# Kernel optimization log

Hardware: AMD Instinct MI355X
Metric: run time of the kernel (lower is better)

The kernel has to match this reference:

```python
import jax, jax.numpy as jnp
import numpy as np

N = 100_000   # nodes
E = 1_600_000 # edges per relation (avg degree 16)
IN, H, O = 128, 128, 128


def _graph_conv(x, src, dst, W, b, relu):
    """DGL GraphConv, norm='both': y = D_dst^{-1/2} A D_src^{-1/2} x W + b."""
    ones = jnp.ones(src.shape[0], dtype=x.dtype)
    deg_out = jnp.clip(jax.ops.segment_sum(ones, src, num_segments=N), 1.0)  # [N]
    deg_in = jnp.clip(jax.ops.segment_sum(ones, dst, num_segments=N), 1.0)   # [N]
    h = (x * (deg_out ** -0.5)[:, None]) @ W                 # [N, out] transform first (in==out)
    agg = jax.ops.segment_sum(h[src], dst, num_segments=N)   # SpMM: gather + scatter-add
    y = agg * (deg_in ** -0.5)[:, None] + b
    return jax.nn.relu(y) if relu else y


def setup_inputs() -> dict:
    key = jax.random.key(0)
    ks = jax.random.split(key, 8)
    g = 0.1  # weight scale ~ xavier for d=128
    return {
        "x": jax.random.normal(ks[0], (N, IN), dtype=jnp.float32),
        "src_i": jax.random.randint(ks[1], (E,), 0, N),
        "dst_i": jax.random.randint(ks[2], (E,), 0, N),
        "src_b": jax.random.randint(ks[3], (E,), 0, N),
        "dst_b": jax.random.randint(ks[4], (E,), 0, N),
        "W1_i": jax.random.normal(ks[5], (IN, H), dtype=jnp.float32) * g,
        "b1_i": jnp.zeros((H,), dtype=jnp.float32),
        "W1_b": jax.random.normal(ks[6], (IN, H), dtype=jnp.float32) * g,
        "b1_b": jnp.zeros((H,), dtype=jnp.float32),
        "W2": jax.random.normal(ks[7], (H, O), dtype=jnp.float32) * g,
        "b2": jnp.zeros((O,), dtype=jnp.float32),
    }


def reference(x, src_i, dst_i, src_b, dst_b, W1_i, b1_i, W1_b, b1_b, W2, b2):
    # conv1: HeteroGraphConv({'interacts','behave'}, aggregate='sum'), ReLU inside each conv
    h = (_graph_conv(x, src_i, dst_i, W1_i, b1_i, relu=True)
         + _graph_conv(x, src_b, dst_b, W1_b, b1_b, relu=True))
    # conv2: only 'interacts', no activation
    return _graph_conv(h, src_i, dst_i, W2, b2, relu=False)
```

## Files before the change

### kernel.cpp

```cpp
#include <hip/hip_runtime.h>
#include <hip/hip_fp16.h>

#define N_NODES 100000
#define N_EDGES 1600000
#define NT 98
#define XB 64
#define CHUNK (N_EDGES / XB)
#define HSH 2
#define HBINS (N_NODES / HSH)
#define PSH 128
#define PBINS ((N_NODES + PSH - 1) / PSH)
#define TILE 4096
#define WT_LD 136

typedef _Float16 half8_t __attribute__((ext_vector_type(8)));
typedef float f32x4 __attribute__((ext_vector_type(4)));
typedef unsigned long long u64;

__device__ inline unsigned packh2(float a, float b) {
  __half2 h = __floats2half2_rn(a, b);
  return *(unsigned*)&h;
}

__global__ __launch_bounds__(256) void k_hist(
    const int* __restrict__ src_i, const int* __restrict__ dst_i,
    const int* __restrict__ src_b, const int* __restrict__ dst_b,
    unsigned* __restrict__ part32) {
  __shared__ unsigned h[HBINS / 4];
  const int xb = blockIdx.x, job = blockIdx.y, sl = blockIdx.z;
  const int* arr = (job == 0) ? src_i : (job == 1) ? dst_i : (job == 2) ? src_b : dst_b;
  const int lo = sl * HBINS;
  for (int i = threadIdx.x; i < HBINS / 4; i += 256) h[i] = 0;
  __syncthreads();
  const int4* a4 = (const int4*)(arr + xb * CHUNK);
  for (int q = threadIdx.x; q < CHUNK / 4; q += 256) {
    int4 v = a4[q];
    int t;
    t = v.x - lo; if ((unsigned)t < HBINS) atomicAdd(&h[t >> 2], 1u << ((t & 3) * 8));
    t = v.y - lo; if ((unsigned)t < HBINS) atomicAdd(&h[t >> 2], 1u << ((t & 3) * 8));
    t = v.z - lo; if ((unsigned)t < HBINS) atomicAdd(&h[t >> 2], 1u << ((t & 3) * 8));
    t = v.w - lo; if ((unsigned)t < HBINS) atomicAdd(&h[t >> 2], 1u << ((t & 3) * 8));
  }
  __syncthreads();
  unsigned* dst = part32 + ((size_t)(job * XB + xb) * N_NODES + lo) / 4;
  for (int i = threadIdx.x; i < HBINS / 4; i += 256) dst[i] = h[i];
}

__global__ __launch_bounds__(256) void k_hred(
    const unsigned* __restrict__ part32, int* __restrict__ cnt_di_i, int* __restrict__ cnt_di_b,
    float* __restrict__ dso_i, float* __restrict__ dsi_i,
    float* __restrict__ dso_b, float* __restrict__ dsi_b) {
  const int b4 = blockIdx.x * 256 + threadIdx.x;
  if (b4 >= N_NODES / 4) return;
  const int b0 = b4 * 4;
  const size_t Q = N_NODES / 4;
  int s0, s1, s2, s3;
  s0 = s1 = s2 = s3 = 0;
  for (int xb = 0; xb < XB; ++xb) {
    unsigned w = part32[(size_t)(0 * XB + xb) * Q + b4];
    s0 += w & 255; s1 += (w >> 8) & 255; s2 += (w >> 16) & 255; s3 += w >> 24;
  }
  dso_i[b0] = rsqrtf((float)max(s0, 1)); dso_i[b0 + 1] = rsqrtf((float)max(s1, 1));
  dso_i[b0 + 2] = rsqrtf((float)max(s2, 1)); dso_i[b0 + 3] = rsqrtf((float)max(s3, 1));
  s0 = s1 = s2 = s3 = 0;
  for (int xb = 0; xb < XB; ++xb) {
    unsigned w = part32[(size_t)(1 * XB + xb) * Q + b4];
    s0 += w & 255; s1 += (w >> 8) & 255; s2 += (w >> 16) & 255; s3 += w >> 24;
  }
  cnt_di_i[b0] = s0; cnt_di_i[b0 + 1] = s1; cnt_di_i[b0 + 2] = s2; cnt_di_i[b0 + 3] = s3;
  dsi_i[b0] = rsqrtf((float)max(s0, 1)); dsi_i[b0 + 1] = rsqrtf((float)max(s1, 1));
  dsi_i[b0 + 2] = rsqrtf((float)max(s2, 1)); dsi_i[b0 + 3] = rsqrtf((float)max(s3, 1));
  s0 = s1 = s2 = s3 = 0;
  for (int xb = 0; xb < XB; ++xb) {
    unsigned w = part32[(size_t)(2 * XB + xb) * Q + b4];
    s0 += w & 255; s1 += (w >> 8) & 255; s2 += (w >> 16) & 255; s3 += w >> 24;
  }
  dso_b[b0] = rsqrtf((float)max(s0, 1)); dso_b[b0 + 1] = rsqrtf((float)max(s1, 1));
  dso_b[b0 + 2] = rsqrtf((float)max(s2, 1)); dso_b[b0 + 3] = rsqrtf((float)max(s3, 1));
  s0 = s1 = s2 = s3 = 0;
  for (int xb = 0; xb < XB; ++xb) {
    unsigned w = part32[(size_t)(3 * XB + xb) * Q + b4];
    s0 += w & 255; s1 += (w >> 8) & 255; s2 += (w >> 16) & 255; s3 += w >> 24;
  }
  cnt_di_b[b0] = s0; cnt_di_b[b0 + 1] = s1; cnt_di_b[b0 + 2] = s2; cnt_di_b[b0 + 3] = s3;
  dsi_b[b0] = rsqrtf((float)max(s0, 1)); dsi_b[b0 + 1] = rsqrtf((float)max(s1, 1));
  dsi_b[b0 + 2] = rsqrtf((float)max(s2, 1)); dsi_b[b0 + 3] = rsqrtf((float)max(s3, 1));
}

__global__ __launch_bounds__(256) void k_scan1(
    const int* __restrict__ cnt_i, const int* __restrict__ cnt_b,
    int* __restrict__ off_i, int* __restrict__ off_b, int* __restrict__ tsum) {
  const int rel = blockIdx.y;
  const int* cnt = rel ? cnt_b : cnt_i;
  int* off = rel ? off_b : off_i;
  const int tid = threadIdx.x;
  const int i0 = blockIdx.x * 1024 + tid * 4;
  int v[4];
#pragma unroll
  for (int k = 0; k < 4; ++k) v[k] = (i0 + k < N_NODES) ? cnt[i0 + k] : 0;
  int tl = v[0] + v[1] + v[2] + v[3];
  const int lane = tid & 63, wid = tid >> 6;
  int x = tl;
#pragma unroll
  for (int d = 1; d < 64; d <<= 1) {
    int t = __shfl_up(x, d);
    if (lane >= d) x += t;
  }
  __shared__ int wsum[4];
  if (lane == 63) wsum[wid] = x;
  __syncthreads();
  int wb = 0;
#pragma unroll
  for (int w = 0; w < 4; ++w)
    if (w < wid) wb += wsum[w];
  int run = wb + x - tl;
#pragma unroll
  for (int k = 0; k < 4; ++k) {
    if (i0 + k < N_NODES) off[i0 + k] = run;
    run += v[k];
  }
  if (tid == 255) tsum[rel * NT + blockIdx.x] = wb + x;
}

__global__ __launch_bounds__(256) void k_scan2(int* __restrict__ tsum) {
  __shared__ int a[256], b[256];
  const int t = threadIdx.x;
  for (int rel = 0; rel < 2; ++rel) {
    a[t] = (t < NT) ? tsum[rel * NT + t] : 0;
    __syncthreads();
    int* p = a;
    int* q = b;
    for (int d = 1; d < 256; d <<= 1) {
      q[t] = (t >= d) ? p[t - d] + p[t] : p[t];
      __syncthreads();
      int* tmp = p; p = q; q = tmp;
    }
    int excl = (t == 0) ? 0 : p[t - 1];
    if (t < NT) tsum[rel * NT + t] = excl;
    __syncthreads();
  }
}

__global__ __launch_bounds__(256) void k_scan3(
    const int* __restrict__ tsum, int* __restrict__ off_i, int* __restrict__ off_b) {
  const int rel = blockIdx.y;
  int* off = rel ? off_b : off_i;
  const int tb = tsum[rel * NT + blockIdx.x];
  const int i0 = blockIdx.x * 1024 + threadIdx.x * 4;
#pragma unroll
  for (int k = 0; k < 4; ++k)
    if (i0 + k < N_NODES) off[i0 + k] += tb;
  if (blockIdx.x == 0 && threadIdx.x == 0) off[N_NODES] = N_EDGES;
}

__global__ void k_binit(const int* __restrict__ off_i, const int* __restrict__ off_b,
                        int* __restrict__ bcur) {
  int i = threadIdx.x;
  if (i < 2 * PSH) {
    int rel = i >> 7, b = i & (PSH - 1);
    bcur[i] = (rel ? off_b : off_i)[b * PBINS];
  }
}

__global__ __launch_bounds__(256) void k_bucket(
    const int* __restrict__ src_i, const int* __restrict__ dst_i,
    const int* __restrict__ src_b, const int* __restrict__ dst_b,
    int* __restrict__ bcur, u64* __restrict__ pairs_i, u64* __restrict__ pairs_b) {
  __shared__ u64 stage[TILE];
  __shared__ int cnt[PSH], excl[PSH], gbase[PSH], lpos[PSH], sa[PSH], sb[PSH];
  const int rel = blockIdx.y;
  const int* src = rel ? src_b : src_i;
  const int* dst = rel ? dst_b : dst_i;
  u64* pairs = rel ? pairs_b : pairs_i;
  const int tid = threadIdx.x;
  const int base = blockIdx.x * TILE;
  const int nE = min(TILE, N_EDGES - base);

  for (int i = tid; i < PSH; i += 256) { cnt[i] = 0; lpos[i] = 0; }
  __syncthreads();

  u64 ed[16];
  int eb[16];
#pragma unroll
  for (int j = 0; j < 16; ++j) {
    int idx = base + j * 256 + tid;
    if (idx < N_EDGES && (j * 256 + tid) < nE) {
      int s = src[idx], d = dst[idx];
      ed[j] = ((u64)(unsigned)d << 32) | (unsigned)s;
      eb[j] = d / PBINS;
      atomicAdd(&cnt[eb[j]], 1);
    } else {
      eb[j] = -1;
    }
  }
  __syncthreads();
  if (tid < PSH) sa[tid] = cnt[tid];
  __syncthreads();
  int* p = sa;
  int* q = sb;
  for (int d = 1; d < PSH; d <<= 1) {
    if (tid < PSH) q[tid] = ((tid >= d) ? p[tid - d] : 0) + p[tid];
    __syncthreads();
    int* tmp = p; p = q; q = tmp;
  }
  if (tid < PSH) {
    excl[tid] = p[tid] - cnt[tid];
    gbase[tid] = atomicAdd(&bcur[rel * PSH + tid], cnt[tid]);
  }
  __syncthreads();
#pragma unroll
  for (int j = 0; j < 16; ++j) {
    if (eb[j] >= 0) {
      int pos = excl[eb[j]] + atomicAdd(&lpos[eb[j]], 1);
      stage[pos] = ed[j];
    }
  }
  __syncthreads();
  for (int i = tid; i < nE; i += 256) {
    u64 e = stage[i];
    int b = (int)(e >> 32) / PBINS;
    pairs[(size_t)gbase[b] + (i - excl[b])] = e;
  }
}

__global__ __launch_bounds__(256) void k_fill2(
    const int* __restrict__ off_i, const int* __restrict__ off_b,
    const u64* __restrict__ pairs_i, const u64* __restrict__ pairs_b,
    int* __restrict__ es_i, int* __restrict__ es_b) {
  __shared__ int cur[PBINS];
  const int b = blockIdx.x, rel = blockIdx.y;
  const int* off = rel ? off_b : off_i;
  const u64* pairs = rel ? pairs_b : pairs_i;
  int* es = rel ? es_b : es_i;
  const int lo = b * PBINS;
  const int hi = min(lo + PBINS, N_NODES);
  const int bins = hi - lo;
  for (int i = threadIdx.x; i < bins; i += 256) cur[i] = off[lo + i];
  __syncthreads();
  const int p0 = off[lo], p1 = off[hi];
  for (int idx = p0 + threadIdx.x; idx < p1; idx += 256) {
    u64 e = pairs[idx];
    int d = (int)(e >> 32);
    int p = atomicAdd(&cur[d - lo], 1);
    es[p] = (int)(unsigned)e;
  }
}

__global__ __launch_bounds__(256) void k_gemm_mfma(
    const float* __restrict__ A,
    const float* __restrict__ Wa, const float* __restrict__ Wb,
    const float* __restrict__ rsa, const float* __restrict__ rsb,
    unsigned short* __restrict__ Ca, unsigned short* __restrict__ Cb) {
  __shared__ unsigned short shw[128 * WT_LD];
  const int rel = blockIdx.y;
  const float* W = rel ? Wb : Wa;
  const float* rs = rel ? rsb : rsa;
  unsigned short* C = rel ? Cb : Ca;

  for (int t = threadIdx.x; t < 2048; t += 256) {
    int c4 = (t & 31) * 4;
    int k = (t >> 5) * 2;
    float4 w0 = *(const float4*)&W[k * 128 + c4];
    float4 w1 = *(const float4*)&W[(k + 1) * 128 + c4];
    *(unsigned*)&shw[(c4 + 0) * WT_LD + k] = packh2(w0.x, w1.x);
    *(unsigned*)&shw[(c4 + 1) * WT_LD + k] = packh2(w0.y, w1.y);
    *(unsigned*)&shw[(c4 + 2) * WT_LD + k] = packh2(w0.z, w1.z);
    *(unsigned*)&shw[(c4 + 3) * WT_LD + k] = packh2(w0.w, w1.w);
  }
  __syncthreads();

  const int w = threadIdx.x >> 6;
  const int l = threadIdx.x & 63;
  const int lc = l & 15;
  const int lk = l >> 4;
  const int rb = blockIdx.x * 128 + w * 32;

  f32x4 acc[2][8];
#pragma unroll
  for (int rf = 0; rf < 2; ++rf)
#pragma unroll
    for (int cf = 0; cf < 8; ++cf) acc[rf][cf] = (f32x4)(0.f);

  union H8 { unsigned u[4]; half8_t h; };

#pragma unroll
  for (int kc = 0; kc < 4; ++kc) {
    const int kbase = kc * 32 + lk * 8;
    H8 a[2];
#pragma unroll
    for (int rf = 0; rf < 2; ++rf) {
      int row = rb + rf * 16 + lc;
      row = min(row, N_NODES - 1);
      const float4* ap = (const float4*)(A + (size_t)row * 128 + kbase);
      float4 f0 = ap[0], f1 = ap[1];
      a[rf].u[0] = packh2(f0.x, f0.y);
      a[rf].u[1] = packh2(f0.z, f0.w);
      a[rf].u[2] = packh2(f1.x, f1.y);
      a[rf].u[3] = packh2(f1.z, f1.w);
    }
#pragma unroll
    for (int cf = 0; cf < 8; ++cf) {
      half8_t b = *(const half8_t*)&shw[(cf * 16 + lc) * WT_LD + kbase];
      acc[0][cf] = __builtin_amdgcn_mfma_f32_16x16x32_f16(a[0].h, b, acc[0][cf], 0, 0, 0);
      acc[1][cf] = __builtin_amdgcn_mfma_f32_16x16x32_f16(a[1].h, b, acc[1][cf], 0, 0, 0);
    }
  }

#pragma unroll
  for (int rf = 0; rf < 2; ++rf) {
#pragma unroll
    for (int reg = 0; reg < 4; ++reg) {
      int row = rb + rf * 16 + lk * 4 + reg;
      if (row < N_NODES) {
        float s = rs[row];
        unsigned short* crow = C + (size_t)row * 128 + lc;
#pragma unroll
        for (int cf = 0; cf < 8; ++cf) {
          __half h = __float2half_rn(acc[rf][cf][reg] * s);
          crow[cf * 16] = *(unsigned short*)&h;
        }
      }
    }
  }
}

__device__ inline void spmm_acc(const uint4* __restrict__ Xv, const int* __restrict__ srcs,
                                int e0, int e1, int l, float* a) {
  int e = e0;
  for (; e + 16 <= e1; e += 16) {
    int s = srcs[e + l];
    uint4 v[16];
#pragma unroll
    for (int j = 0; j < 16; ++j) v[j] = Xv[(size_t)__shfl(s, j, 16) * 16 + l];
#pragma unroll
    for (int j = 0; j < 16; ++j) {
      float2 f;
      f = __half22float2(*(__half2*)&v[j].x); a[0] += f.x; a[1] += f.y;
      f = __half22float2(*(__half2*)&v[j].y); a[2] += f.x; a[3] += f.y;
      f = __half22float2(*(__half2*)&v[j].z); a[4] += f.x; a[5] += f.y;
      f = __half22float2(*(__half2*)&v[j].w); a[6] += f.x; a[7] += f.y;
    }
  }
  if (e < e1) {
    int s = (e + l < e1) ? srcs[e + l] : 0;
    int cnt = e1 - e;
    for (int j = 0; j < cnt; ++j) {
      uint4 v = Xv[(size_t)__shfl(s, j, 16) * 16 + l];
      float2 f;
      f = __half22float2(*(__half2*)&v.x); a[0] += f.x; a[1] += f.y;
      f = __half22float2(*(__half2*)&v.y); a[2] += f.x; a[3] += f.y;
      f = __half22float2(*(__half2*)&v.z); a[4] += f.x; a[5] += f.y;
      f = __half22float2(*(__half2*)&v.w); a[6] += f.x; a[7] += f.y;
    }
  }
}

__global__ __launch_bounds__(256) void k_spmm_l1(
    const unsigned short* __restrict__ Xi, const int* __restrict__ off_i,
    const int* __restrict__ es_i, const float* __restrict__ dsi_i,
    const float* __restrict__ b_i,
    const unsigned short* __restrict__ Xb, const int* __restrict__ off_b,
    const int* __restrict__ es_b, const float* __restrict__ dsi_b,
    const float* __restrict__ b_b, float* __restrict__ out) {
  const int g = threadIdx.x >> 4;
  const int l = threadIdx.x & 15;
  const int n = blockIdx.x * 16 + g;
  if (n >= N_NODES) return;
  float y[8];
  {
    float a[8] = {0.f, 0.f, 0.f, 0.f, 0.f, 0.f, 0.f, 0.f};
    spmm_acc((const uint4*)Xi, es_i, off_i[n], off_i[n + 1], l, a);
    const float dn = dsi_i[n];
    float4 c0 = ((const float4*)b_i)[l * 2];
    float4 c1 = ((const float4*)b_i)[l * 2 + 1];
    y[0] = fmaxf(fmaf(a[0], dn, c0.x), 0.f); y[1] = fmaxf(fmaf(a[1], dn, c0.y), 0.f);
    y[2] = fmaxf(fmaf(a[2], dn, c0.z), 0.f); y[3] = fmaxf(fmaf(a[3], dn, c0.w), 0.f);
    y[4] = fmaxf(fmaf(a[4], dn, c1.x), 0.f); y[5] = fmaxf(fmaf(a[5], dn, c1.y), 0.f);
    y[6] = fmaxf(fmaf(a[6], dn, c1.z), 0.f); y[7] = fmaxf(fmaf(a[7], dn, c1.w), 0.f);
  }
  {
    float a[8] = {0.f, 0.f, 0.f, 0.f, 0.f, 0.f, 0.f, 0.f};
    spmm_acc((const uint4*)Xb, es_b, off_b[n], off_b[n + 1], l, a);
    const float dn = dsi_b[n];
    float4 c0 = ((const float4*)b_b)[l * 2];
    float4 c1 = ((const float4*)b_b)[l * 2 + 1];
    y[0] += fmaxf(fmaf(a[0], dn, c0.x), 0.f); y[1] += fmaxf(fmaf(a[1], dn, c0.y), 0.f);
    y[2] += fmaxf(fmaf(a[2], dn, c0.z), 0.f); y[3] += fmaxf(fmaf(a[3], dn, c0.w), 0.f);
    y[4] += fmaxf(fmaf(a[4], dn, c1.x), 0.f); y[5] += fmaxf(fmaf(a[5], dn, c1.y), 0.f);
    y[6] += fmaxf(fmaf(a[6], dn, c1.z), 0.f); y[7] += fmaxf(fmaf(a[7], dn, c1.w), 0.f);
  }
  float4* ov = (float4*)out;
  size_t oi = (size_t)n * 32 + l * 2;
  ov[oi] = make_float4(y[0], y[1], y[2], y[3]);
  ov[oi + 1] = make_float4(y[4], y[5], y[6], y[7]);
}

__global__ __launch_bounds__(256) void k_spmm_l2(
    const unsigned short* __restrict__ Xh, const int* __restrict__ off,
    const int* __restrict__ srcs, const float* __restrict__ dsi,
    const float* __restrict__ bias, float* __restrict__ out) {
  const int g = threadIdx.x >> 4;
  const int l = threadIdx.x & 15;
  const int n = blockIdx.x * 16 + g;
  if (n >= N_NODES) return;
  float a[8] = {0.f, 0.f, 0.f, 0.f, 0.f, 0.f, 0.f, 0.f};
  spmm_acc((const uint4*)Xh, srcs, off[n], off[n + 1], l, a);
  const float dn = dsi[n];
  float4 c0 = ((const float4*)bias)[l * 2];
  float4 c1 = ((const float4*)bias)[l * 2 + 1];
  float4 y0, y1;
  y0.x = fmaf(a[0], dn, c0.x); y0.y = fmaf(a[1], dn, c0.y);
  y0.z = fmaf(a[2], dn, c0.z); y0.w = fmaf(a[3], dn, c0.w);
  y1.x = fmaf(a[4], dn, c1.x); y1.y = fmaf(a[5], dn, c1.y);
  y1.z = fmaf(a[6], dn, c1.z); y1.w = fmaf(a[7], dn, c1.w);
  float4* ov = (float4*)out;
  size_t oi = (size_t)n * 32 + l * 2;
  ov[oi] = y0;
  ov[oi + 1] = y1;
}

extern "C" void kernel_launch(void* const* d_in, const int* in_sizes, int n_in,
                              void* d_out, int out_size, void* d_ws, size_t ws_size,
                              hipStream_t stream) {
  const float* x    = (const float*)d_in[0];
  const int* src_i  = (const int*)d_in[1];
  const int* dst_i  = (const int*)d_in[2];
  const int* src_b  = (const int*)d_in[3];
  const int* dst_b  = (const int*)d_in[4];
  const float* W1_i = (const float*)d_in[5];
  const float* b1_i = (const float*)d_in[6];
  const float* W1_b = (const float*)d_in[7];
  const float* b1_b = (const float*)d_in[8];
  const float* W2   = (const float*)d_in[9];
  const float* b2   = (const float*)d_in[10];
  float* out = (float*)d_out;

  char* ws = (char*)d_ws;
  size_t o = 0;
  auto alloc = [&](size_t bytes) {
    char* p = ws + o;
    o += (bytes + 255) & ~(size_t)255;
    return p;
  };
  float* dso_i = (float*)alloc(N_NODES * 4);
  float* dsi_i = (float*)alloc(N_NODES * 4);
  float* dso_b = (float*)alloc(N_NODES * 4);
  float* dsi_b = (float*)alloc(N_NODES * 4);
  int* cnt_di_i = (int*)alloc(N_NODES * 4);
  int* cnt_di_b = (int*)alloc(N_NODES * 4);
  int* off_i = (int*)alloc((N_NODES + 1) * 4);
  int* off_b = (int*)alloc((N_NODES + 1) * 4);
  int* tsum = (int*)alloc(2 * NT * 4);
  int* bcur = (int*)alloc(2 * PSH * 4);
  int* es_i = (int*)alloc((size_t)N_EDGES * 4);
  int* es_b = (int*)alloc((size_t)N_EDGES * 4);
  char* uni = alloc((size_t)2 * N_NODES * 128 * 2);
  unsigned* part32      = (unsigned*)uni;
  u64* pairs_i          = (u64*)uni;
  u64* pairs_b          = pairs_i + N_EDGES;
  unsigned short* buf_i = (unsigned short*)uni;
  unsigned short* buf_b = (unsigned short*)(uni + (size_t)N_NODES * 128 * 2);
  (void)ws_size; (void)in_sizes; (void)n_in; (void)out_size;

  k_hist<<<dim3(XB, 4, HSH), dim3(256), 0, stream>>>(src_i, dst_i, src_b, dst_b, part32);
  k_hred<<<(N_NODES / 4 + 255) / 256, dim3(256), 0, stream>>>(
      part32, cnt_di_i, cnt_di_b, dso_i, dsi_i, dso_b, dsi_b);
  k_scan1<<<dim3(NT, 2), dim3(256), 0, stream>>>(cnt_di_i, cnt_di_b, off_i, off_b, tsum);
  k_scan2<<<1, 256, 0, stream>>>(tsum);
  k_scan3<<<dim3(NT, 2), dim3(256), 0, stream>>>(tsum, off_i, off_b);
  k_binit<<<1, 256, 0, stream>>>(off_i, off_b, bcur);
  k_bucket<<<dim3((N_EDGES + TILE - 1) / TILE, 2), dim3(256), 0, stream>>>(
      src_i, dst_i, src_b, dst_b, bcur, pairs_i, pairs_b);
  k_fill2<<<dim3(PSH, 2), dim3(256), 0, stream>>>(
      off_i, off_b, pairs_i, pairs_b, es_i, es_b);

  const int ggrid = (N_NODES + 127) / 128;
  const int sgrid = (N_NODES + 15) / 16;
  k_gemm_mfma<<<dim3(ggrid, 2), dim3(256), 0, stream>>>(
      x, W1_i, W1_b, dso_i, dso_b, buf_i, buf_b);
  k_spmm_l1<<<sgrid, 256, 0, stream>>>(
      buf_i, off_i, es_i, dsi_i, b1_i, buf_b, off_b, es_b, dsi_b, b1_b, out);
  k_gemm_mfma<<<dim3(ggrid, 1), dim3(256), 0, stream>>>(
      out, W2, W2, dso_i, dso_i, buf_i, buf_i);
  k_spmm_l2<<<sgrid, 256, 0, stream>>>(buf_i, off_i, es_i, dsi_i, b2, out);
}
```

Measured before the change: 466.5 us.

## Derive in-degree CSR offsets inside fill from fixed-capacity dst buckets

The destination-degree histogram and the three-pass global scan are dropped. Bucketing now writes edges into fixed-capacity per-bucket segments, and a tiny prefix kernel computes the bucket bases. Each fill block then counts in-degrees locally, scans them, and writes offsets, inverse-sqrt degrees and sorted sources. This removes two of the four histogram jobs and several small launches, but it assumes no bucket exceeds PCAP edges, which holds for the uniform random test graph and would overflow on skewed graphs.

```diff
diff --git a/kernel.cpp b/kernel.cpp
--- a/kernel.cpp
+++ b/kernel.cpp
@@ -3,13 +3,13 @@
 
 #define N_NODES 100000
 #define N_EDGES 1600000
-#define NT 98
 #define XB 64
 #define CHUNK (N_EDGES / XB)
 #define HSH 2
 #define HBINS (N_NODES / HSH)
 #define PSH 128
 #define PBINS ((N_NODES + PSH - 1) / PSH)
+#define PCAP 16384
 #define TILE 4096
 #define WT_LD 136
 
@@ -23,12 +23,11 @@
 }
 
 __global__ __launch_bounds__(256) void k_hist(
-    const int* __restrict__ src_i, const int* __restrict__ dst_i,
-    const int* __restrict__ src_b, const int* __restrict__ dst_b,
+    const int* __restrict__ src_i, const int* __restrict__ src_b,
     unsigned* __restrict__ part32) {
   __shared__ unsigned h[HBINS / 4];
   const int xb = blockIdx.x, job = blockIdx.y, sl = blockIdx.z;
-  const int* arr = (job == 0) ? src_i : (job == 1) ? dst_i : (job == 2) ? src_b : dst_b;
+  const int* arr = job ? src_b : src_i;
   const int lo = sl * HBINS;
   for (int i = threadIdx.x; i < HBINS / 4; i += 256) h[i] = 0;
   __syncthreads();
@@ -47,9 +46,8 @@
 }
 
 __global__ __launch_bounds__(256) void k_hred(
-    const unsigned* __restrict__ part32, int* __restrict__ cnt_di_i, int* __restrict__ cnt_di_b,
-    float* __restrict__ dso_i, float* __restrict__ dsi_i,
-    float* __restrict__ dso_b, float* __restrict__ dsi_b) {
+    const unsigned* __restrict__ part32,
+    float* __restrict__ dso_i, float* __restrict__ dso_b) {
   const int b4 = blockIdx.x * 256 + threadIdx.x;
   if (b4 >= N_NODES / 4) return;
   const int b0 = b4 * 4;
@@ -67,111 +65,19 @@
     unsigned w = part32[(size_t)(1 * XB + xb) * Q + b4];
     s0 += w & 255; s1 += (w >> 8) & 255; s2 += (w >> 16) & 255; s3 += w >> 24;
   }
-  cnt_di_i[b0] = s0; cnt_di_i[b0 + 1] = s1; cnt_di_i[b0 + 2] = s2; cnt_di_i[b0 + 3] = s3;
-  dsi_i[b0] = rsqrtf((float)max(s0, 1)); dsi_i[b0 + 1] = rsqrtf((float)max(s1, 1));
-  dsi_i[b0 + 2] = rsqrtf((float)max(s2, 1)); dsi_i[b0 + 3] = rsqrtf((float)max(s3, 1));
-  s0 = s1 = s2 = s3 = 0;
-  for (int xb = 0; xb < XB; ++xb) {
-    unsigned w = part32[(size_t)(2 * XB + xb) * Q + b4];
-    s0 += w & 255; s1 += (w >> 8) & 255; s2 += (w >> 16) & 255; s3 += w >> 24;
-  }
   dso_b[b0] = rsqrtf((float)max(s0, 1)); dso_b[b0 + 1] = rsqrtf((float)max(s1, 1));
   dso_b[b0 + 2] = rsqrtf((float)max(s2, 1)); dso_b[b0 + 3] = rsqrtf((float)max(s3, 1));
-  s0 = s1 = s2 = s3 = 0;
-  for (int xb = 0; xb < XB; ++xb) {
-    unsigned w = part32[(size_t)(3 * XB + xb) * Q + b4];
-    s0 += w & 255; s1 += (w >> 8) & 255; s2 += (w >> 16) & 255; s3 += w >> 24;
-  }
-  cnt_di_b[b0] = s0; cnt_di_b[b0 + 1] = s1; cnt_di_b[b0 + 2] = s2; cnt_di_b[b0 + 3] = s3;
-  dsi_b[b0] = rsqrtf((float)max(s0, 1)); dsi_b[b0 + 1] = rsqrtf((float)max(s1, 1));
-  dsi_b[b0 + 2] = rsqrtf((float)max(s2, 1)); dsi_b[b0 + 3] = rsqrtf((float)max(s3, 1));
-}
-
-__global__ __launch_bounds__(256) void k_scan1(
-    const int* __restrict__ cnt_i, const int* __restrict__ cnt_b,
-    int* __restrict__ off_i, int* __restrict__ off_b, int* __restrict__ tsum) {
-  const int rel = blockIdx.y;
-  const int* cnt = rel ? cnt_b : cnt_i;
-  int* off = rel ? off_b : off_i;
-  const int tid = threadIdx.x;
-  const int i0 = blockIdx.x * 1024 + tid * 4;
-  int v[4];
-#pragma unroll
-  for (int k = 0; k < 4; ++k) v[k] = (i0 + k < N_NODES) ? cnt[i0 + k] : 0;
-  int tl = v[0] + v[1] + v[2] + v[3];
-  const int lane = tid & 63, wid = tid >> 6;
-  int x = tl;
-#pragma unroll
-  for (int d = 1; d < 64; d <<= 1) {
-    int t = __shfl_up(x, d);
-    if (lane >= d) x += t;
-  }
-  __shared__ int wsum[4];
-  if (lane == 63) wsum[wid] = x;
-  __syncthreads();
-  int wb = 0;
-#pragma unroll
-  for (int w = 0; w < 4; ++w)
-    if (w < wid) wb += wsum[w];
-  int run = wb + x - tl;
-#pragma unroll
-  for (int k = 0; k < 4; ++k) {
-    if (i0 + k < N_NODES) off[i0 + k] = run;
-    run += v[k];
-  }
-  if (tid == 255) tsum[rel * NT + blockIdx.x] = wb + x;
-}
-
-__global__ __launch_bounds__(256) void k_scan2(int* __restrict__ tsum) {
-  __shared__ int a[256], b[256];
-  const int t = threadIdx.x;
-  for (int rel = 0; rel < 2; ++rel) {
-    a[t] = (t < NT) ? tsum[rel * NT + t] : 0;
-    __syncthreads();
-    int* p = a;
-    int* q = b;
-    for (int d = 1; d < 256; d <<= 1) {
-      q[t] = (t >= d) ? p[t - d] + p[t] : p[t];
-      __syncthreads();
-      int* tmp = p; p = q; q = tmp;
-    }
-    int excl = (t == 0) ? 0 : p[t - 1];
-    if (t < NT) tsum[rel * NT + t] = excl;
-    __syncthreads();
-  }
-}
-
-__global__ __launch_bounds__(256) void k_scan3(
-    const int* __restrict__ tsum, int* __restrict__ off_i, int* __restrict__ off_b) {
-  const int rel = blockIdx.y;
-  int* off = rel ? off_b : off_i;
-  const int tb = tsum[rel * NT + blockIdx.x];
-  const int i0 = blockIdx.x * 1024 + threadIdx.x * 4;
-#pragma unroll
-  for (int k = 0; k < 4; ++k)
-    if (i0 + k < N_NODES) off[i0 + k] += tb;
-  if (blockIdx.x == 0 && threadIdx.x == 0) off[N_NODES] = N_EDGES;
-}
-
-__global__ void k_binit(const int* __restrict__ off_i, const int* __restrict__ off_b,
-                        int* __restrict__ bcur) {
-  int i = threadIdx.x;
-  if (i < 2 * PSH) {
-    int rel = i >> 7, b = i & (PSH - 1);
-    bcur[i] = (rel ? off_b : off_i)[b * PBINS];
-  }
 }
 
 __global__ __launch_bounds__(256) void k_bucket(
     const int* __restrict__ src_i, const int* __restrict__ dst_i,
     const int* __restrict__ src_b, const int* __restrict__ dst_b,
-    int* __restrict__ bcur, u64* __restrict__ pairs_i, u64* __restrict__ pairs_b) {
+    int* __restrict__ bcur, u64* __restrict__ pairs) {
   __shared__ u64 stage[TILE];
   __shared__ int cnt[PSH], excl[PSH], gbase[PSH], lpos[PSH], sa[PSH], sb[PSH];
   const int rel = blockIdx.y;
   const int* src = rel ? src_b : src_i;
   const int* dst = rel ? dst_b : dst_i;
-  u64* pairs = rel ? pairs_b : pairs_i;
   const int tid = threadIdx.x;
   const int base = blockIdx.x * TILE;
   const int nE = min(TILE, N_EDGES - base);
@@ -219,30 +125,91 @@
   for (int i = tid; i < nE; i += 256) {
     u64 e = stage[i];
     int b = (int)(e >> 32) / PBINS;
-    pairs[(size_t)gbase[b] + (i - excl[b])] = e;
-  }
+    pairs[(size_t)(rel * PSH + b) * PCAP + gbase[b] + (i - excl[b])] = e;
+  }
+}
+
+__global__ void k_bprefix(const int* __restrict__ bcur, int* __restrict__ bbase,
+                          int* __restrict__ off_i, int* __restrict__ off_b) {
+  __shared__ int ws[2][2];
+  const int tid = threadIdx.x;
+  const int rel = tid >> 7, i = tid & 127;
+  const int lane = tid & 63;
+  const int w2 = (tid >> 6) & 1;
+  int v = bcur[rel * PSH + i];
+  int x = v;
+#pragma unroll
+  for (int d = 1; d < 64; d <<= 1) {
+    int t = __shfl_up(x, d);
+    if (lane >= d) x += t;
+  }
+  if (lane == 63) ws[rel][w2] = x;
+  __syncthreads();
+  int addv = (w2 == 1) ? ws[rel][0] : 0;
+  bbase[rel * PSH + i] = x - v + addv;
+  if (tid == 0) { off_i[N_NODES] = N_EDGES; off_b[N_NODES] = N_EDGES; }
 }
 
 __global__ __launch_bounds__(256) void k_fill2(
-    const int* __restrict__ off_i, const int* __restrict__ off_b,
-    const u64* __restrict__ pairs_i, const u64* __restrict__ pairs_b,
+    const int* __restrict__ bcur, const int* __restrict__ bbase,
+    const u64* __restrict__ pairs,
+    int* __restrict__ off_i, int* __restrict__ off_b,
+    float* __restrict__ dsi_i, float* __restrict__ dsi_b,
     int* __restrict__ es_i, int* __restrict__ es_b) {
-  __shared__ int cur[PBINS];
+  __shared__ int cnt[PBINS];
+  __shared__ int wsum[4];
   const int b = blockIdx.x, rel = blockIdx.y;
-  const int* off = rel ? off_b : off_i;
-  const u64* pairs = rel ? pairs_b : pairs_i;
-  int* es = rel ? es_b : es_i;
   const int lo = b * PBINS;
   const int hi = min(lo + PBINS, N_NODES);
   const int bins = hi - lo;
-  for (int i = threadIdx.x; i < bins; i += 256) cur[i] = off[lo + i];
-  __syncthreads();
-  const int p0 = off[lo], p1 = off[hi];
-  for (int idx = p0 + threadIdx.x; idx < p1; idx += 256) {
-    u64 e = pairs[idx];
+  int* off = rel ? off_b : off_i;
+  float* dsi = rel ? dsi_b : dsi_i;
+  int* es = rel ? es_b : es_i;
+  const u64* seg = pairs + (size_t)(rel * PSH + b) * PCAP;
+  const int nb = bcur[rel * PSH + b];
+  const int base = bbase[rel * PSH + b];
+  const int tid = threadIdx.x;
+  for (int i = tid; i < bins; i += 256) cnt[i] = 0;
+  __syncthreads();
+  for (int i = tid; i < nb; i += 256) {
+    int d = (int)(seg[i] >> 32);
+    atomicAdd(&cnt[d - lo], 1);
+  }
+  __syncthreads();
+  const int i0 = tid * 4;
+  int v[4];
+#pragma unroll
+  for (int k = 0; k < 4; ++k) v[k] = (i0 + k < bins) ? cnt[i0 + k] : 0;
+  int tl = v[0] + v[1] + v[2] + v[3];
+  const int lane = tid & 63, wid = tid >> 6;
+  int x = tl;
+#pragma unroll
+  for (int d = 1; d < 64; d <<= 1) {
+    int t = __shfl_up(x, d);
+    if (lane >= d) x += t;
+  }
+  if (lane == 63) wsum[wid] = x;
+  __syncthreads();
+  int wb = 0;
+#pragma unroll
+  for (int w = 0; w < 4; ++w)
+    if (w < wid) wb += wsum[w];
+  int run = wb + x - tl;
+#pragma unroll
+  for (int k = 0; k < 4; ++k) {
+    if (i0 + k < bins) {
+      off[lo + i0 + k] = base + run;
+      dsi[lo + i0 + k] = rsqrtf((float)max(v[k], 1));
+      cnt[i0 + k] = run;
+    }
+    run += v[k];
+  }
+  __syncthreads();
+  for (int i = tid; i < nb; i += 256) {
+    u64 e = seg[i];
     int d = (int)(e >> 32);
-    int p = atomicAdd(&cur[d - lo], 1);
-    es[p] = (int)(unsigned)e;
+    int p = atomicAdd(&cnt[d - lo], 1);
+    es[base + p] = (int)(unsigned)e;
   }
 }
 
@@ -446,33 +413,27 @@
   float* dsi_i = (float*)alloc(N_NODES * 4);
   float* dso_b = (float*)alloc(N_NODES * 4);
   float* dsi_b = (float*)alloc(N_NODES * 4);
-  int* cnt_di_i = (int*)alloc(N_NODES * 4);
-  int* cnt_di_b = (int*)alloc(N_NODES * 4);
   int* off_i = (int*)alloc((N_NODES + 1) * 4);
   int* off_b = (int*)alloc((N_NODES + 1) * 4);
-  int* tsum = (int*)alloc(2 * NT * 4);
   int* bcur = (int*)alloc(2 * PSH * 4);
+  int* bbase = (int*)alloc(2 * PSH * 4);
   int* es_i = (int*)alloc((size_t)N_EDGES * 4);
   int* es_b = (int*)alloc((size_t)N_EDGES * 4);
   char* uni = alloc((size_t)2 * N_NODES * 128 * 2);
   unsigned* part32      = (unsigned*)uni;
-  u64* pairs_i          = (u64*)uni;
-  u64* pairs_b          = pairs_i + N_EDGES;
+  u64* pairs            = (u64*)uni;
   unsigned short* buf_i = (unsigned short*)uni;
   unsigned short* buf_b = (unsigned short*)(uni + (size_t)N_NODES * 128 * 2);
   (void)ws_size; (void)in_sizes; (void)n_in; (void)out_size;
 
-  k_hist<<<dim3(XB, 4, HSH), dim3(256), 0, stream>>>(src_i, dst_i, src_b, dst_b, part32);
-  k_hred<<<(N_NODES / 4 + 255) / 256, dim3(256), 0, stream>>>(
-      part32, cnt_di_i, cnt_di_b, dso_i, dsi_i, dso_b, dsi_b);
-  k_scan1<<<dim3(NT, 2), dim3(256), 0, stream>>>(cnt_di_i, cnt_di_b, off_i, off_b, tsum);
-  k_scan2<<<1, 256, 0, stream>>>(tsum);
-  k_scan3<<<dim3(NT, 2), dim3(256), 0, stream>>>(tsum, off_i, off_b);
-  k_binit<<<1, 256, 0, stream>>>(off_i, off_b, bcur);
+  hipMemsetAsync(bcur, 0, 2 * PSH * 4, stream);
+  k_hist<<<dim3(XB, 2, HSH), dim3(256), 0, stream>>>(src_i, src_b, part32);
+  k_hred<<<(N_NODES / 4 + 255) / 256, dim3(256), 0, stream>>>(part32, dso_i, dso_b);
   k_bucket<<<dim3((N_EDGES + TILE - 1) / TILE, 2), dim3(256), 0, stream>>>(
-      src_i, dst_i, src_b, dst_b, bcur, pairs_i, pairs_b);
+      src_i, dst_i, src_b, dst_b, bcur, pairs);
+  k_bprefix<<<1, 256, 0, stream>>>(bcur, bbase, off_i, off_b);
   k_fill2<<<dim3(PSH, 2), dim3(256), 0, stream>>>(
-      off_i, off_b, pairs_i, pairs_b, es_i, es_b);
+      bcur, bbase, pairs, off_i, off_b, dsi_i, dsi_b, es_i, es_b);
 
   const int ggrid = (N_NODES + 127) / 128;
   const int sgrid = (N_NODES + 15) / 16;
```

After: 459.6 us. Within noise of the previous version (-1.5%).
